# Performance work log

Hardware: AMD Instinct MI355X
Metric: run time of the kernel (lower is better)

The kernel has to match this reference:

```python
import jax, jax.numpy as jnp
import numpy as np

D_MODEL = 768
NUM_HEADS = 12


def setup_inputs() -> dict:
    key = jax.random.key(0)
    ks = jax.random.split(key, 11)
    B, N, D = 4, 2048, D_MODEL
    s = 1.0 / np.sqrt(D)
    return {
        "q": jax.random.normal(ks[0], (B, N, D), jnp.float32),
        "k": jax.random.normal(ks[1], (B, N, D), jnp.float32),
        "v": jax.random.normal(ks[2], (B, N, D), jnp.float32),
        "wq": jax.random.normal(ks[3], (D, D), jnp.float32) * s,
        "bq": jnp.zeros((D,), jnp.float32),
        "wk": jax.random.normal(ks[4], (D, D), jnp.float32) * s,
        "bk": jnp.zeros((D,), jnp.float32),
        "wv": jax.random.normal(ks[5], (D, D), jnp.float32) * s,
        "bv": jnp.zeros((D,), jnp.float32),
        "wo": jax.random.normal(ks[6], (D, D), jnp.float32) * s,
        "bo": jnp.zeros((D,), jnp.float32),
    }


def _split_heads(x, num_heads):
    B, N, D = x.shape
    hd = D // num_heads
    return x.reshape(B, N, num_heads, hd).transpose(0, 2, 1, 3)  # (B,H,N,hd)


def reference(q, k, v, wq, bq, wk, bk, wv, bv, wo, bo):
    B, N, D = q.shape
    H = NUM_HEADS
    qw = q @ wq.T + bq
    kw = k @ wk.T + bk
    vw = v @ wv.T + bv
    hq = _split_heads(qw, H)
    hk = _split_heads(kw, H)
    hv = _split_heads(vw, H)
    scale = 1.0 / jnp.sqrt(jnp.asarray(hq.shape[-1], hq.dtype))
    scores = jnp.einsum("bhnd,bhmd->bhnm", hq, hk) * scale  # (B,H,N,N) explicit
    attn = jax.nn.softmax(scores, axis=-1)
    out = jnp.einsum("bhnm,bhmd->bhnd", attn, hv)
    out = out.transpose(0, 2, 1, 3).reshape(B, N, D)
    return out @ wo.T + bo
```

## Files before the change

### kernel.cpp

```cpp
#include <hip/hip_runtime.h>
#include <hip/hip_bf16.h>
#include <type_traits>


typedef __attribute__((ext_vector_type(8)))  __bf16 bf16x8;
typedef __attribute__((ext_vector_type(4)))  __bf16 bf16x4;
typedef __attribute__((ext_vector_type(4)))  float  f32x4;
typedef __attribute__((ext_vector_type(16))) float  f32x16;
typedef __attribute__((ext_vector_type(2)))  unsigned u32x2;
typedef __attribute__((ext_vector_type(4)))  unsigned u32x4;

#define NH  12
#define HD  64
#define DM  768
#define SEQ 2048
#define NB  4
#define M8  8192
#define ALPHA 0.18033688011112043f

__device__ __forceinline__ f32x4 mfma16(bf16x8 a, bf16x8 b, f32x4 c) {
  return __builtin_amdgcn_mfma_f32_16x16x32_bf16(a, b, c, 0, 0, 0);
}
__device__ __forceinline__ f32x16 mfma32(bf16x8 a, bf16x8 b, f32x16 c) {
  return __builtin_amdgcn_mfma_f32_32x32x16_bf16(a, b, c, 0, 0, 0);
}
__device__ __forceinline__ void gload16(const void* g, void* l) {
  auto gp = (__attribute__((address_space(1))) void*)(const_cast<void*>(g));
  auto lp = (__attribute__((address_space(3))) void*)(l);
  __builtin_amdgcn_global_load_lds(gp, lp, 16, 0, 0);
}
__device__ __forceinline__ float exp2_(float x) {
#if __has_builtin(__builtin_amdgcn_exp2f)
  return __builtin_amdgcn_exp2f(x);
#else
  return exp2f(x);
#endif
}

#define VMLG(n) do { asm volatile("s_waitcnt vmcnt(" #n ") lgkmcnt(0)" ::: "memory"); \
                     __builtin_amdgcn_sched_barrier(0); } while (0)
#define VMW(n) do { asm volatile("s_waitcnt vmcnt(" #n ")" ::: "memory"); \
                    __builtin_amdgcn_sched_barrier(0); } while (0)
#define BARX do { __builtin_amdgcn_s_barrier(); \
                  __builtin_amdgcn_sched_barrier(0); } while (0)

__device__ __forceinline__ u32x2 pswap(unsigned a, unsigned b) {
#if __has_builtin(__builtin_amdgcn_permlane32_swap)
  return __builtin_amdgcn_permlane32_swap(a, b, false, false);
#else
  u32x2 r;
  unsigned sa = (unsigned)__shfl_xor((int)a, 32), sb = (unsigned)__shfl_xor((int)b, 32);
  int hi = ((int)threadIdx.x >> 5) & 1;
  r[0] = hi ? sb : a;
  r[1] = hi ? b : sa;
  return r;
#endif
}
__device__ __forceinline__ unsigned f2u(float x) { return __builtin_bit_cast(unsigned, x); }
__device__ __forceinline__ float    u2f(unsigned x) { return __builtin_bit_cast(float, x); }
__device__ __forceinline__ float pcomb_sum(float v) {
  u32x2 r = pswap(f2u(v), f2u(v));
  return u2f(r[0]) + u2f(r[1]);
}
__device__ __forceinline__ unsigned pk(float lo, float hi_) {
  unsigned short ua = __builtin_bit_cast(unsigned short, (__bf16)lo);
  unsigned short ub = __builtin_bit_cast(unsigned short, (__bf16)hi_);
  return ((unsigned)ub << 16) | ua;
}

__global__ void cast4_kernel(const float* __restrict__ a, const float* __restrict__ b,
                             const float* __restrict__ c, const float* __restrict__ d,
                             __bf16* __restrict__ oa, __bf16* __restrict__ ob,
                             __bf16* __restrict__ oc, __bf16* __restrict__ od, int n4) {
  int y = blockIdx.y;
  const float* in = y == 0 ? a : y == 1 ? b : y == 2 ? c : d;
  __bf16* out     = y == 0 ? oa : y == 1 ? ob : y == 2 ? oc : od;
  const float sc  = y == 0 ? ALPHA : 1.0f;
  int i = blockIdx.x * 256 + threadIdx.x;
  if (i < n4) {
    float4 v = ((const float4*)in)[i];
    bf16x4 r;
    r[0] = (__bf16)(v.x * sc); r[1] = (__bf16)(v.y * sc);
    r[2] = (__bf16)(v.z * sc); r[3] = (__bf16)(v.w * sc);
    ((bf16x4*)out)[i] = r;
  }
}

__device__ __forceinline__ void proj_body(const float* __restrict__ A,
                                          const __bf16* __restrict__ B,
                                          const float* __restrict__ bias,
                                          __bf16* __restrict__ C,
                                          long m0, long n0, float bscale, bool trans) {
  __shared__ __align__(16) char LDSG[32768];
  const int tid = threadIdx.x;
  const int w = tid >> 6, l = tid & 63;
  const int g = l >> 4, i16 = l & 15;
  const int wr = w >> 1, wc = w & 1;
  const int srow = l >> 2;
  const int kq = l & 3;
  const int swc = kq ^ ((srow >> 1) & 3);

  const __bf16* Bg = B + (n0 + 16 * w + srow) * (long)DM + swc * 8;
  const float*  Ag = A + (m0 + 16 * w + srow) * (long)DM + kq * 8;
  char* const Awr = LDSG + w * 1024 + srow * 64 + swc * 16;

  const int chsw = (g ^ ((i16 >> 1) & 3)) * 16;
  const char* fA = LDSG + (wr * 64 + i16) * 64 + chsw;
  const char* fB = LDSG + 16384 + (wc * 64 + i16) * 64 + chsw;

  f32x4 acc[4][4] = {};
  float4 arA[4], arB[4];
  long kAa = 0, kAb = 32, kB = 0;

  auto LAA = [&]() {
    arA[0] = *(const float4*)(Ag + kAa);
    arA[1] = *(const float4*)(Ag + kAa + 4);
    arA[2] = *(const float4*)(Ag + 64 * (long)DM + kAa);
    arA[3] = *(const float4*)(Ag + 64 * (long)DM + kAa + 4);
    kAa += 64;
  };
  auto LAB = [&]() {
    arB[0] = *(const float4*)(Ag + kAb);
    arB[1] = *(const float4*)(Ag + kAb + 4);
    arB[2] = *(const float4*)(Ag + 64 * (long)DM + kAb);
    arB[3] = *(const float4*)(Ag + 64 * (long)DM + kAb + 4);
    kAb += 64;
  };
  auto SB = [&](int selb) {
    gload16(Bg + kB, LDSG + 16384 + selb + w * 1024);
    gload16(Bg + 64 * (long)DM + kB, LDSG + 16384 + selb + w * 1024 + 4096);
    kB += 32;
  };
  auto WAA = [&](int selb) {
    u32x4 u0, u1;
    u0[0] = pk(arA[0].x, arA[0].y); u0[1] = pk(arA[0].z, arA[0].w);
    u0[2] = pk(arA[1].x, arA[1].y); u0[3] = pk(arA[1].z, arA[1].w);
    u1[0] = pk(arA[2].x, arA[2].y); u1[1] = pk(arA[2].z, arA[2].w);
    u1[2] = pk(arA[3].x, arA[3].y); u1[3] = pk(arA[3].z, arA[3].w);
    *(u32x4*)(Awr + selb) = u0;
    *(u32x4*)(Awr + selb + 4096) = u1;
  };
  auto WAB = [&](int selb) {
    u32x4 u0, u1;
    u0[0] = pk(arB[0].x, arB[0].y); u0[1] = pk(arB[0].z, arB[0].w);
    u0[2] = pk(arB[1].x, arB[1].y); u0[3] = pk(arB[1].z, arB[1].w);
    u1[0] = pk(arB[2].x, arB[2].y); u1[1] = pk(arB[2].z, arB[2].w);
    u1[2] = pk(arB[3].x, arB[3].y); u1[3] = pk(arB[3].z, arB[3].w);
    *(u32x4*)(Awr + selb) = u0;
    *(u32x4*)(Awr + selb + 4096) = u1;
  };

#define PCOMPUTE(SELB) do { \
    bf16x8 af[4], bfr[4]; \
    _Pragma("unroll") for (int m = 0; m < 4; ++m) \
      af[m] = *(const bf16x8*)(fA + (SELB) + m * 1024); \
    _Pragma("unroll") for (int n = 0; n < 4; ++n) \
      bfr[n] = *(const bf16x8*)(fB + (SELB) + n * 1024); \
    __builtin_amdgcn_s_setprio(1); \
    _Pragma("unroll") for (int m = 0; m < 4; ++m) \
      _Pragma("unroll") for (int n = 0; n < 4; ++n) \
        acc[m][n] = mfma16(af[m], bfr[n], acc[m][n]); \
    __builtin_amdgcn_s_setprio(0); } while (0)

  SB(0); LAA(); LAB(); WAA(0);
  asm volatile("s_waitcnt lgkmcnt(0)" ::: "memory");
  __builtin_amdgcn_sched_barrier(0);
  BARX;
#pragma unroll 1
  for (int j = 0; j < 11; ++j) {
    SB(8192); LAA(); PCOMPUTE(0);    WAB(8192); VMLG(4); BARX;
    SB(0);    LAB(); PCOMPUTE(8192); WAA(0);    VMLG(4); BARX;
  }
  SB(8192); PCOMPUTE(0); WAB(8192); VMLG(0); BARX;
  PCOMPUTE(8192);
#undef PCOMPUTE

  if (trans) {
#pragma unroll
    for (int m = 0; m < 4; ++m)
#pragma unroll
      for (int n = 0; n < 4; ++n) {
        const long col = n0 + wc * 64 + n * 16 + i16;
        const float bv = bias[col] * bscale;
        const long row0 = m0 + wr * 64 + m * 16 + g * 4;
        bf16x4 v4;
#pragma unroll
        for (int r = 0; r < 4; ++r) v4[r] = (__bf16)(acc[m][n][r] + bv);
        *(bf16x4*)(C + col * (long)M8 + row0) = v4;
      }
  } else {
#pragma unroll
    for (int m = 0; m < 4; ++m)
#pragma unroll
      for (int n = 0; n < 4; ++n) {
        const long col = n0 + wc * 64 + n * 16 + i16;
        const float bv = bias[col] * bscale;
        const long row0 = m0 + wr * 64 + m * 16 + g * 4;
#pragma unroll
        for (int r = 0; r < 4; ++r)
          C[(row0 + r) * DM + col] = (__bf16)(acc[m][n][r] + bv);
      }
  }
}

__global__ __launch_bounds__(256, 3) void proj3_gemm(
    const float* __restrict__ q, const float* __restrict__ k, const float* __restrict__ v,
    const __bf16* __restrict__ wqb, const __bf16* __restrict__ wkb, const __bf16* __restrict__ wvb,
    const float* __restrict__ bq, const float* __restrict__ bk, const float* __restrict__ bv,
    __bf16* __restrict__ qpj, __bf16* __restrict__ kpj, __bf16* __restrict__ vpT) {
  const int gid = blockIdx.x;
  const int swz = (gid & 7) * 144 + (gid >> 3);
  const int z = swz / 384, rem = swz % 384;
  const long xb = rem / 6, yb = rem % 6;
  const float* A = z == 0 ? q : z == 1 ? k : v;
  const __bf16* B = z == 0 ? wqb : z == 1 ? wkb : wvb;
  const float* bias = z == 0 ? bq : z == 1 ? bk : bv;
  __bf16* C = z == 0 ? qpj : z == 1 ? kpj : vpT;
  proj_body(A, B, bias, C, xb * 128, yb * 128, z == 0 ? ALPHA : 1.0f, z == 2);
}

__global__ __launch_bounds__(256) void out_gemm(const __bf16* __restrict__ A,
                                                const __bf16* __restrict__ B,
                                                const float* __restrict__ bias,
                                                float* __restrict__ C) {
  const int gid = blockIdx.x;
  const int swz = (gid & 7) * 48 + (gid >> 3);
  const long m0 = (swz / 6) * 128, n0 = (swz % 6) * 128;

  __shared__ __align__(16) char LDSG[32768];
  const int tid = threadIdx.x;
  const int w = tid >> 6, l = tid & 63;
  const int g = l >> 4, i16 = l & 15;
  const int wr = w >> 1, wc = w & 1;
  const int srow = l >> 2;
  const int swc = (l & 3) ^ ((srow >> 1) & 3);
  const __bf16* Ag = A + (m0 + 16 * w + srow) * (long)DM + swc * 8;
  const __bf16* Bg = B + (n0 + 16 * w + srow) * (long)DM + swc * 8;
  const int chsw = (g ^ ((i16 >> 1) & 3)) * 16;
  const char* fA = LDSG + (wr * 64 + i16) * 64 + chsw;
  const char* fB = LDSG + 16384 + (wc * 64 + i16) * 64 + chsw;

  f32x4 acc[4][4] = {};
  long kB = 0;

#define GSTAGE(SELB) do { \
    gload16(Ag + kB, LDSG + (SELB) + w * 1024); \
    gload16(Ag + 64 * (long)DM + kB, LDSG + (SELB) + w * 1024 + 4096); \
    gload16(Bg + kB, LDSG + 16384 + (SELB) + w * 1024); \
    gload16(Bg + 64 * (long)DM + kB, LDSG + 16384 + (SELB) + w * 1024 + 4096); \
    kB += 32; } while (0)

#define GCOMPUTE(SELB) do { \
    bf16x8 af[4], bfr[4]; \
    _Pragma("unroll") for (int m = 0; m < 4; ++m) \
      af[m] = *(const bf16x8*)(fA + (SELB) + m * 1024); \
    _Pragma("unroll") for (int n = 0; n < 4; ++n) \
      bfr[n] = *(const bf16x8*)(fB + (SELB) + n * 1024); \
    __builtin_amdgcn_s_setprio(1); \
    _Pragma("unroll") for (int m = 0; m < 4; ++m) \
      _Pragma("unroll") for (int n = 0; n < 4; ++n) \
        acc[m][n] = mfma16(af[m], bfr[n], acc[m][n]); \
    __builtin_amdgcn_s_setprio(0); } while (0)

  GSTAGE(0); GSTAGE(8192);
#pragma unroll 1
  for (int k = 0; k + 128 <= DM; k += 64) {
    VMW(4); BARX; GCOMPUTE(0);    BARX; GSTAGE(0);
    VMW(4); BARX; GCOMPUTE(8192); BARX; GSTAGE(8192);
  }
  VMW(4); BARX; GCOMPUTE(0);
  VMW(0); BARX; GCOMPUTE(8192);
#undef GSTAGE
#undef GCOMPUTE

#pragma unroll
  for (int m = 0; m < 4; ++m)
#pragma unroll
    for (int n = 0; n < 4; ++n) {
      const long col = n0 + wc * 64 + n * 16 + i16;
      const float bv = bias[col];
      const long row0 = m0 + wr * 64 + m * 16 + g * 4;
#pragma unroll
      for (int r = 0; r < 4; ++r)
        C[(row0 + r) * DM + col] = acc[m][n][r] + bv;
    }
}

__global__ __launch_bounds__(256) void attn_fwd(const __bf16* __restrict__ qp,
                                                const __bf16* __restrict__ kp,
                                                const __bf16* __restrict__ vpT,
                                                __bf16* __restrict__ ao) {
  __shared__ __align__(16) __bf16 Ks[2][64 * 64];
  __shared__ __align__(16) __bf16 Vs[2][64 * 64];

  const int wg = blockIdx.x;
  const int xcd = wg & 7;
  const int idx = wg >> 3;
  const int bh = xcd * 6 + (idx >> 4);
  const int qt = idx & 15;
  const int b = bh / NH, h = bh % NH;

  const int tid = threadIdx.x;
  const int w = tid >> 6, l = tid & 63;
  const int l31 = l & 31, hi = l >> 5;

  const long qrow = (long)b * SEQ + qt * 128 + w * 32 + l31;
  const __bf16* qb = qp + qrow * DM + h * HD;
  bf16x8 qf[4];
#pragma unroll
  for (int kk = 0; kk < 4; ++kk) qf[kk] = *(const bf16x8*)(qb + kk * 16 + hi * 8);

  f32x16 o0 = {}, o1 = {};
  float lsum = 0.f;

  const int srow = tid >> 3;
  const int schunk = (tid & 7) ^ (srow & 7);
  const __bf16* kbase = kp + ((long)b * SEQ) * DM + h * HD;
  const __bf16* vtb = vpT + (long)(h * HD) * M8 + (long)b * SEQ;

  auto stage = [&](int T, int sel) {
    const long kt = (long)T * 64;
    __bf16* Kd = &Ks[sel][(w * 8) * 64];
    __bf16* Vd = &Vs[sel][(w * 8) * 64];
    gload16(kbase + (kt + srow) * (long)DM + schunk * 8, Kd);
    gload16(kbase + (kt + 32 + srow) * (long)DM + schunk * 8, Kd + 32 * 64);
    gload16(vtb + (long)srow * M8 + kt + schunk * 8, Vd);
    gload16(vtb + (long)(32 + srow) * M8 + kt + schunk * 8, Vd + 32 * 64);
  };

  auto compute = [&](const __bf16* Kc, const __bf16* Vc) {
    f32x16 s0 = {}, s1 = {};
    __builtin_amdgcn_s_setprio(1);
#pragma unroll
    for (int kk = 0; kk < 4; ++kk) {
      const int cl = kk * 2 + hi;
      bf16x8 kf0 = *(const bf16x8*)&Kc[l31 * 64 + ((cl ^ (l31 & 7)) * 8)];
      s0 = mfma32(kf0, qf[kk], s0);
      bf16x8 kf1 = *(const bf16x8*)&Kc[(32 + l31) * 64 + ((cl ^ (l31 & 7)) * 8)];
      s1 = mfma32(kf1, qf[kk], s1);
    }
    __builtin_amdgcn_s_setprio(0);

#pragma unroll
    for (int r = 0; r < 16; ++r) s0[r] = exp2_(s0[r]);
#pragma unroll
    for (int r = 0; r < 16; ++r) s1[r] = exp2_(s1[r]);
    f32x16 ps = s0 + s1;
    const float t0 = (ps[0] + ps[1]) + (ps[2] + ps[3]);
    const float t1 = (ps[4] + ps[5]) + (ps[6] + ps[7]);
    const float t2 = (ps[8] + ps[9]) + (ps[10] + ps[11]);
    const float t3 = (ps[12] + ps[13]) + (ps[14] + ps[15]);
    lsum += (t0 + t1) + (t2 + t3);

    bf16x8 pf[4];
#pragma unroll
    for (int ks = 0; ks < 4; ++ks) {
      const int base = 8 * (ks & 1);
      const f32x16& S = (ks < 2) ? s0 : s1;
      unsigned pa = pk(S[base + 0], S[base + 1]);
      unsigned pc = pk(S[base + 2], S[base + 3]);
      unsigned pb = pk(S[base + 4], S[base + 5]);
      unsigned pd = pk(S[base + 6], S[base + 7]);
      u32x2 r02 = pswap(pa, pb);
      u32x2 r13 = pswap(pc, pd);
      u32x4 pw;
      pw[0] = r02[0]; pw[1] = r13[0]; pw[2] = r02[1]; pw[3] = r13[1];
      pf[ks] = __builtin_bit_cast(bf16x8, pw);
    }

    __builtin_amdgcn_s_setprio(1);
#pragma unroll
    for (int ks = 0; ks < 4; ++ks) {
      const int cl = ks * 2 + hi;
      bf16x8 vf0 = *(const bf16x8*)&Vc[l31 * 64 + ((cl ^ (l31 & 7)) * 8)];
      o0 = mfma32(vf0, pf[ks], o0);
      bf16x8 vf1 = *(const bf16x8*)&Vc[(32 + l31) * 64 + ((cl ^ (l31 & 7)) * 8)];
      o1 = mfma32(vf1, pf[ks], o1);
    }
    __builtin_amdgcn_s_setprio(0);
  };

  stage(0, 0);
  __syncthreads();
  for (int t = 0; t < SEQ / 64; t += 2) {
    if (t + 1 < SEQ / 64) stage(t + 1, 1);
    compute(Ks[0], Vs[0]);
    __syncthreads();
    if (t + 2 < SEQ / 64) stage(t + 2, 0);
    compute(Ks[1], Vs[1]);
    __syncthreads();
  }

  const float inv = 1.0f / pcomb_sum(lsum);
  __bf16* obase = ao + qrow * DM + h * HD;
#pragma unroll
  for (int rg = 0; rg < 4; ++rg) {
    bf16x4 v0, v1;
#pragma unroll
    for (int j = 0; j < 4; ++j) {
      v0[j] = (__bf16)(o0[rg * 4 + j] * inv);
      v1[j] = (__bf16)(o1[rg * 4 + j] * inv);
    }
    *(bf16x4*)(obase + 8 * rg + 4 * hi) = v0;
    *(bf16x4*)(obase + 32 + 8 * rg + 4 * hi) = v1;
  }
}

extern "C" void kernel_launch(void* const* d_in, const int* in_sizes, int n_in,
                              void* d_out, int out_size, void* d_ws, size_t ws_size,
                              hipStream_t stream) {
  const float* q  = (const float*)d_in[0];
  const float* k  = (const float*)d_in[1];
  const float* v  = (const float*)d_in[2];
  const float* wq = (const float*)d_in[3];
  const float* bq = (const float*)d_in[4];
  const float* wk = (const float*)d_in[5];
  const float* bk = (const float*)d_in[6];
  const float* wv = (const float*)d_in[7];
  const float* bv = (const float*)d_in[8];
  const float* wo = (const float*)d_in[9];
  const float* bo = (const float*)d_in[10];

  const long S = (long)M8 * DM;
  const long W = (long)DM * DM;
  __bf16* ws = (__bf16*)d_ws;
  __bf16 *wqb = ws, *wkb = wqb + W, *wvb = wkb + W, *wob = wvb + W;
  __bf16 *qpj = wob + W, *kpj = qpj + S, *vpT = kpj + S, *aob = vpT + S;

  cast4_kernel<<<dim3((unsigned)(W / 4 / 256), 4), 256, 0, stream>>>(
      wq, wk, wv, wo, wqb, wkb, wvb, wob, (int)(W / 4));

  proj3_gemm<<<1152, 256, 0, stream>>>(q, k, v, wqb, wkb, wvb, bq, bk, bv, qpj, kpj, vpT);

  attn_fwd<<<768, 256, 0, stream>>>(qpj, kpj, vpT, aob);

  out_gemm<<<384, 256, 0, stream>>>(aob, wob, bo, (float*)d_out);
}
```

Measured before the change: 153.2 us.

## Give each attention wave two 32-row query tiles, halving threads per block

The attention kernel now runs 2 waves of 128 threads per block instead of 4. Each wave handles 64 query rows as two 32-row MFMA tiles that share each K and V fragment read from LDS, which halves the LDS reads per MFMA. The staging loop is reworked so 128 threads still fill the same 64x64 K/V tiles. The cost is roughly double the accumulator and score registers per wave and fewer waves per block to hide latency.

Measured after the change: 152.9 us. About the same (-0.2%).

```diff
diff --git a/kernel.cpp b/kernel.cpp
--- a/kernel.cpp
+++ b/kernel.cpp
@@ -286,10 +286,10 @@
     }
 }
 
-__global__ __launch_bounds__(256) void attn_fwd(const __bf16* __restrict__ qp,
-                                                const __bf16* __restrict__ kp,
-                                                const __bf16* __restrict__ vpT,
-                                                __bf16* __restrict__ ao) {
+__global__ __launch_bounds__(128, 2) void attn_fwd(const __bf16* __restrict__ qp,
+                                                   const __bf16* __restrict__ kp,
+                                                   const __bf16* __restrict__ vpT,
+                                                   __bf16* __restrict__ ao) {
   __shared__ __align__(16) __bf16 Ks[2][64 * 64];
   __shared__ __align__(16) __bf16 Vs[2][64 * 64];
 
@@ -304,14 +304,17 @@
   const int w = tid >> 6, l = tid & 63;
   const int l31 = l & 31, hi = l >> 5;
 
-  const long qrow = (long)b * SEQ + qt * 128 + w * 32 + l31;
-  const __bf16* qb = qp + qrow * DM + h * HD;
-  bf16x8 qf[4];
-#pragma unroll
-  for (int kk = 0; kk < 4; ++kk) qf[kk] = *(const bf16x8*)(qb + kk * 16 + hi * 8);
-
-  f32x16 o0 = {}, o1 = {};
-  float lsum = 0.f;
+  const long qrow0 = (long)b * SEQ + qt * 128 + w * 64 + l31;
+  const __bf16* qb0 = qp + qrow0 * DM + h * HD;
+  bf16x8 qf0[4], qf1[4];
+#pragma unroll
+  for (int kk = 0; kk < 4; ++kk) {
+    qf0[kk] = *(const bf16x8*)(qb0 + kk * 16 + hi * 8);
+    qf1[kk] = *(const bf16x8*)(qb0 + 32 * DM + kk * 16 + hi * 8);
+  }
+
+  f32x16 o00 = {}, o01 = {}, o10 = {}, o11 = {};
+  float lsum0 = 0.f, lsum1 = 0.f;
 
   const int srow = tid >> 3;
   const int schunk = (tid & 7) ^ (srow & 7);
@@ -320,62 +323,95 @@
 
   auto stage = [&](int T, int sel) {
     const long kt = (long)T * 64;
-    __bf16* Kd = &Ks[sel][(w * 8) * 64];
-    __bf16* Vd = &Vs[sel][(w * 8) * 64];
-    gload16(kbase + (kt + srow) * (long)DM + schunk * 8, Kd);
-    gload16(kbase + (kt + 32 + srow) * (long)DM + schunk * 8, Kd + 32 * 64);
-    gload16(vtb + (long)srow * M8 + kt + schunk * 8, Vd);
-    gload16(vtb + (long)(32 + srow) * M8 + kt + schunk * 8, Vd + 32 * 64);
+    __bf16* Kd = &Ks[sel][w * 512];
+    __bf16* Vd = &Vs[sel][w * 512];
+#pragma unroll
+    for (int j = 0; j < 4; ++j) {
+      gload16(kbase + (kt + 16 * j + srow) * (long)DM + schunk * 8, Kd + j * 1024);
+      gload16(vtb + (long)(16 * j + srow) * M8 + kt + schunk * 8, Vd + j * 1024);
+    }
   };
 
   auto compute = [&](const __bf16* Kc, const __bf16* Vc) {
-    f32x16 s0 = {}, s1 = {};
+    f32x16 s00 = {}, s01 = {}, s10 = {}, s11 = {};
     __builtin_amdgcn_s_setprio(1);
 #pragma unroll
     for (int kk = 0; kk < 4; ++kk) {
-      const int cl = kk * 2 + hi;
-      bf16x8 kf0 = *(const bf16x8*)&Kc[l31 * 64 + ((cl ^ (l31 & 7)) * 8)];
-      s0 = mfma32(kf0, qf[kk], s0);
-      bf16x8 kf1 = *(const bf16x8*)&Kc[(32 + l31) * 64 + ((cl ^ (l31 & 7)) * 8)];
-      s1 = mfma32(kf1, qf[kk], s1);
+      const int sw = ((kk * 2 + hi) ^ (l31 & 7)) * 8;
+      bf16x8 kf0 = *(const bf16x8*)&Kc[l31 * 64 + sw];
+      s00 = mfma32(kf0, qf0[kk], s00);
+      s10 = mfma32(kf0, qf1[kk], s10);
+      bf16x8 kf1 = *(const bf16x8*)&Kc[2048 + l31 * 64 + sw];
+      s01 = mfma32(kf1, qf0[kk], s01);
+      s11 = mfma32(kf1, qf1[kk], s11);
     }
     __builtin_amdgcn_s_setprio(0);
 
 #pragma unroll
-    for (int r = 0; r < 16; ++r) s0[r] = exp2_(s0[r]);
-#pragma unroll
-    for (int r = 0; r < 16; ++r) s1[r] = exp2_(s1[r]);
-    f32x16 ps = s0 + s1;
-    const float t0 = (ps[0] + ps[1]) + (ps[2] + ps[3]);
-    const float t1 = (ps[4] + ps[5]) + (ps[6] + ps[7]);
-    const float t2 = (ps[8] + ps[9]) + (ps[10] + ps[11]);
-    const float t3 = (ps[12] + ps[13]) + (ps[14] + ps[15]);
-    lsum += (t0 + t1) + (t2 + t3);
-
-    bf16x8 pf[4];
+    for (int r = 0; r < 16; ++r) s00[r] = exp2_(s00[r]);
+#pragma unroll
+    for (int r = 0; r < 16; ++r) s01[r] = exp2_(s01[r]);
+#pragma unroll
+    for (int r = 0; r < 16; ++r) s10[r] = exp2_(s10[r]);
+#pragma unroll
+    for (int r = 0; r < 16; ++r) s11[r] = exp2_(s11[r]);
+    {
+      f32x16 ps = s00 + s01;
+      const float t0 = (ps[0] + ps[1]) + (ps[2] + ps[3]);
+      const float t1 = (ps[4] + ps[5]) + (ps[6] + ps[7]);
+      const float t2 = (ps[8] + ps[9]) + (ps[10] + ps[11]);
+      const float t3 = (ps[12] + ps[13]) + (ps[14] + ps[15]);
+      lsum0 += (t0 + t1) + (t2 + t3);
+    }
+    {
+      f32x16 ps = s10 + s11;
+      const float t0 = (ps[0] + ps[1]) + (ps[2] + ps[3]);
+      const float t1 = (ps[4] + ps[5]) + (ps[6] + ps[7]);
+      const float t2 = (ps[8] + ps[9]) + (ps[10] + ps[11]);
+      const float t3 = (ps[12] + ps[13]) + (ps[14] + ps[15]);
+      lsum1 += (t0 + t1) + (t2 + t3);
+    }
+
+    bf16x8 pf0[4], pf1[4];
 #pragma unroll
     for (int ks = 0; ks < 4; ++ks) {
       const int base = 8 * (ks & 1);
-      const f32x16& S = (ks < 2) ? s0 : s1;
-      unsigned pa = pk(S[base + 0], S[base + 1]);
-      unsigned pc = pk(S[base + 2], S[base + 3]);
-      unsigned pb = pk(S[base + 4], S[base + 5]);
-      unsigned pd = pk(S[base + 6], S[base + 7]);
-      u32x2 r02 = pswap(pa, pb);
-      u32x2 r13 = pswap(pc, pd);
-      u32x4 pw;
-      pw[0] = r02[0]; pw[1] = r13[0]; pw[2] = r02[1]; pw[3] = r13[1];
-      pf[ks] = __builtin_bit_cast(bf16x8, pw);
+      {
+        const f32x16& S = (ks < 2) ? s00 : s01;
+        unsigned pa = pk(S[base + 0], S[base + 1]);
+        unsigned pc = pk(S[base + 2], S[base + 3]);
+        unsigned pb = pk(S[base + 4], S[base + 5]);
+        unsigned pd = pk(S[base + 6], S[base + 7]);
+        u32x2 r02 = pswap(pa, pb);
+        u32x2 r13 = pswap(pc, pd);
+        u32x4 pw;
+        pw[0] = r02[0]; pw[1] = r13[0]; pw[2] = r02[1]; pw[3] = r13[1];
+        pf0[ks] = __builtin_bit_cast(bf16x8, pw);
+      }
+      {
+        const f32x16& S = (ks < 2) ? s10 : s11;
+        unsigned pa = pk(S[base + 0], S[base + 1]);
+        unsigned pc = pk(S[base + 2], S[base + 3]);
+        unsigned pb = pk(S[base + 4], S[base + 5]);
+        unsigned pd = pk(S[base + 6], S[base + 7]);
+        u32x2 r02 = pswap(pa, pb);
+        u32x2 r13 = pswap(pc, pd);
+        u32x4 pw;
+        pw[0] = r02[0]; pw[1] = r13[0]; pw[2] = r02[1]; pw[3] = r13[1];
+        pf1[ks] = __builtin_bit_cast(bf16x8, pw);
+      }
     }
 
     __builtin_amdgcn_s_setprio(1);
 #pragma unroll
     for (int ks = 0; ks < 4; ++ks) {
-      const int cl = ks * 2 + hi;
-      bf16x8 vf0 = *(const bf16x8*)&Vc[l31 * 64 + ((cl ^ (l31 & 7)) * 8)];
-      o0 = mfma32(vf0, pf[ks], o0);
-      bf16x8 vf1 = *(const bf16x8*)&Vc[(32 + l31) * 64 + ((cl ^ (l31 & 7)) * 8)];
-      o1 = mfma32(vf1, pf[ks], o1);
+      const int sw = ((ks * 2 + hi) ^ (l31 & 7)) * 8;
+      bf16x8 vf0 = *(const bf16x8*)&Vc[l31 * 64 + sw];
+      o00 = mfma32(vf0, pf0[ks], o00);
+      o10 = mfma32(vf0, pf1[ks], o10);
+      bf16x8 vf1 = *(const bf16x8*)&Vc[2048 + l31 * 64 + sw];
+      o01 = mfma32(vf1, pf0[ks], o01);
+      o11 = mfma32(vf1, pf1[ks], o11);
     }
     __builtin_amdgcn_s_setprio(0);
   };
@@ -391,18 +427,24 @@
     __syncthreads();
   }
 
-  const float inv = 1.0f / pcomb_sum(lsum);
-  __bf16* obase = ao + qrow * DM + h * HD;
+  const float inv0 = 1.0f / pcomb_sum(lsum0);
+  const float inv1 = 1.0f / pcomb_sum(lsum1);
+  __bf16* ob0 = ao + qrow0 * DM + h * HD;
+  __bf16* ob1 = ob0 + 32 * DM;
 #pragma unroll
   for (int rg = 0; rg < 4; ++rg) {
-    bf16x4 v0, v1;
+    bf16x4 a0, a1, b0, b1;
 #pragma unroll
     for (int j = 0; j < 4; ++j) {
-      v0[j] = (__bf16)(o0[rg * 4 + j] * inv);
-      v1[j] = (__bf16)(o1[rg * 4 + j] * inv);
-    }
-    *(bf16x4*)(obase + 8 * rg + 4 * hi) = v0;
-    *(bf16x4*)(obase + 32 + 8 * rg + 4 * hi) = v1;
+      a0[j] = (__bf16)(o00[rg * 4 + j] * inv0);
+      a1[j] = (__bf16)(o01[rg * 4 + j] * inv0);
+      b0[j] = (__bf16)(o10[rg * 4 + j] * inv1);
+      b1[j] = (__bf16)(o11[rg * 4 + j] * inv1);
+    }
+    *(bf16x4*)(ob0 + 8 * rg + 4 * hi) = a0;
+    *(bf16x4*)(ob0 + 32 + 8 * rg + 4 * hi) = a1;
+    *(bf16x4*)(ob1 + 8 * rg + 4 * hi) = b0;
+    *(bf16x4*)(ob1 + 32 + 8 * rg + 4 * hi) = b1;
   }
 }
 
@@ -432,7 +474,7 @@
 
   proj3_gemm<<<1152, 256, 0, stream>>>(q, k, v, wqb, wkb, wvb, bq, bk, bv, qpj, kpj, vpT);
 
-  attn_fwd<<<768, 256, 0, stream>>>(qpj, kpj, vpT, aob);
+  attn_fwd<<<768, 128, 0, stream>>>(qpj, kpj, vpT, aob);
 
   out_gemm<<<384, 256, 0, stream>>>(aob, wob, bo, (float*)d_out);
 }
```

## Software-pipeline PV matmul with next QK in attention; shrink out-GEMM tiles

Applied to the files above, without the earlier changes.

The attention loop is restructured so that the PV MFMAs for tile t-1 run in the same MFMA block as the QK MFMAs for tile t. This interleaves matrix work with the exp/pack softmax step, and V fragments are held in registers across iterations. A launch-bounds occupancy hint of 3 waves is added. The output GEMM switches to 64x128 tiles with 768 blocks to fill more CUs, at the cost of less reuse per block. Keeping extra fragments live raises register pressure, which may conflict with the occupancy target.

After: 148.5 us (median of 2 runs). 1.03x faster.

```diff
diff --git a/kernel.cpp b/kernel.cpp
--- a/kernel.cpp
+++ b/kernel.cpp
@@ -224,10 +224,12 @@
                                                 const float* __restrict__ bias,
                                                 float* __restrict__ C) {
   const int gid = blockIdx.x;
-  const int swz = (gid & 7) * 48 + (gid >> 3);
-  const long m0 = (swz / 6) * 128, n0 = (swz % 6) * 128;
-
-  __shared__ __align__(16) char LDSG[32768];
+  const int local = (gid >> 3);
+  const long mt = (gid & 7) * 16 + local / 6;
+  const long nt = local % 6;
+  const long m0 = mt * 64, n0 = nt * 128;
+
+  __shared__ __align__(16) char LDSG[24576];
   const int tid = threadIdx.x;
   const int w = tid >> 6, l = tid & 63;
   const int g = l >> 4, i16 = l & 15;
@@ -237,59 +239,58 @@
   const __bf16* Ag = A + (m0 + 16 * w + srow) * (long)DM + swc * 8;
   const __bf16* Bg = B + (n0 + 16 * w + srow) * (long)DM + swc * 8;
   const int chsw = (g ^ ((i16 >> 1) & 3)) * 16;
-  const char* fA = LDSG + (wr * 64 + i16) * 64 + chsw;
-  const char* fB = LDSG + 16384 + (wc * 64 + i16) * 64 + chsw;
-
-  f32x4 acc[4][4] = {};
+  const char* fA = LDSG + (wr * 32 + i16) * 64 + chsw;
+  const char* fB = LDSG + 8192 + (wc * 64 + i16) * 64 + chsw;
+
+  f32x4 acc[2][4] = {};
   long kB = 0;
 
-#define GSTAGE(SELB) do { \
-    gload16(Ag + kB, LDSG + (SELB) + w * 1024); \
-    gload16(Ag + 64 * (long)DM + kB, LDSG + (SELB) + w * 1024 + 4096); \
-    gload16(Bg + kB, LDSG + 16384 + (SELB) + w * 1024); \
-    gload16(Bg + 64 * (long)DM + kB, LDSG + 16384 + (SELB) + w * 1024 + 4096); \
+#define GSTAGE(S) do { \
+    gload16(Ag + kB, LDSG + (S) * 4096 + w * 1024); \
+    gload16(Bg + kB, LDSG + 8192 + (S) * 8192 + w * 1024); \
+    gload16(Bg + 64 * (long)DM + kB, LDSG + 8192 + (S) * 8192 + w * 1024 + 4096); \
     kB += 32; } while (0)
 
-#define GCOMPUTE(SELB) do { \
-    bf16x8 af[4], bfr[4]; \
-    _Pragma("unroll") for (int m = 0; m < 4; ++m) \
-      af[m] = *(const bf16x8*)(fA + (SELB) + m * 1024); \
+#define GCOMPUTE(S) do { \
+    bf16x8 af[2], bfr[4]; \
+    _Pragma("unroll") for (int m = 0; m < 2; ++m) \
+      af[m] = *(const bf16x8*)(fA + (S) * 4096 + m * 1024); \
     _Pragma("unroll") for (int n = 0; n < 4; ++n) \
-      bfr[n] = *(const bf16x8*)(fB + (SELB) + n * 1024); \
+      bfr[n] = *(const bf16x8*)(fB + (S) * 8192 + n * 1024); \
     __builtin_amdgcn_s_setprio(1); \
-    _Pragma("unroll") for (int m = 0; m < 4; ++m) \
+    _Pragma("unroll") for (int m = 0; m < 2; ++m) \
       _Pragma("unroll") for (int n = 0; n < 4; ++n) \
         acc[m][n] = mfma16(af[m], bfr[n], acc[m][n]); \
     __builtin_amdgcn_s_setprio(0); } while (0)
 
-  GSTAGE(0); GSTAGE(8192);
+  GSTAGE(0); GSTAGE(1);
 #pragma unroll 1
   for (int k = 0; k + 128 <= DM; k += 64) {
-    VMW(4); BARX; GCOMPUTE(0);    BARX; GSTAGE(0);
-    VMW(4); BARX; GCOMPUTE(8192); BARX; GSTAGE(8192);
-  }
-  VMW(4); BARX; GCOMPUTE(0);
-  VMW(0); BARX; GCOMPUTE(8192);
+    VMW(3); BARX; GCOMPUTE(0); BARX; GSTAGE(0);
+    VMW(3); BARX; GCOMPUTE(1); BARX; GSTAGE(1);
+  }
+  VMW(3); BARX; GCOMPUTE(0);
+  VMW(0); BARX; GCOMPUTE(1);
 #undef GSTAGE
 #undef GCOMPUTE
 
 #pragma unroll
-  for (int m = 0; m < 4; ++m)
+  for (int m = 0; m < 2; ++m)
 #pragma unroll
     for (int n = 0; n < 4; ++n) {
       const long col = n0 + wc * 64 + n * 16 + i16;
       const float bv = bias[col];
-      const long row0 = m0 + wr * 64 + m * 16 + g * 4;
+      const long row0 = m0 + wr * 32 + m * 16 + g * 4;
 #pragma unroll
       for (int r = 0; r < 4; ++r)
         C[(row0 + r) * DM + col] = acc[m][n][r] + bv;
     }
 }
 
-__global__ __launch_bounds__(256) void attn_fwd(const __bf16* __restrict__ qp,
-                                                const __bf16* __restrict__ kp,
-                                                const __bf16* __restrict__ vpT,
-                                                __bf16* __restrict__ ao) {
+__global__ __launch_bounds__(256, 3) void attn_fwd(const __bf16* __restrict__ qp,
+                                                   const __bf16* __restrict__ kp,
+                                                   const __bf16* __restrict__ vpT,
+                                                   __bf16* __restrict__ ao) {
   __shared__ __align__(16) __bf16 Ks[2][64 * 64];
   __shared__ __align__(16) __bf16 Vs[2][64 * 64];
 
@@ -312,6 +313,7 @@
 
   f32x16 o0 = {}, o1 = {};
   float lsum = 0.f;
+  bf16x8 vfp[8], pfp[4];
 
   const int srow = tid >> 3;
   const int schunk = (tid & 7) ^ (srow & 7);
@@ -328,19 +330,40 @@
     gload16(vtb + (long)(32 + srow) * M8 + kt + schunk * 8, Vd + 32 * 64);
   };
 
-  auto compute = [&](const __bf16* Kc, const __bf16* Vc) {
-    f32x16 s0 = {}, s1 = {};
+  auto qk = [&](const __bf16* Kc, f32x16& s0, f32x16& s1, bool pv) {
+    bf16x8 kf[8];
+#pragma unroll
+    for (int kk = 0; kk < 4; ++kk) {
+      const int sw = ((kk * 2 + hi) ^ (l31 & 7)) * 8;
+      kf[kk]     = *(const bf16x8*)&Kc[l31 * 64 + sw];
+      kf[4 + kk] = *(const bf16x8*)&Kc[2048 + l31 * 64 + sw];
+    }
     __builtin_amdgcn_s_setprio(1);
+    if (pv) {
+#pragma unroll
+      for (int ks = 0; ks < 4; ++ks) {
+        o0 = mfma32(vfp[ks], pfp[ks], o0);
+        o1 = mfma32(vfp[4 + ks], pfp[ks], o1);
+      }
+    }
 #pragma unroll
     for (int kk = 0; kk < 4; ++kk) {
-      const int cl = kk * 2 + hi;
-      bf16x8 kf0 = *(const bf16x8*)&Kc[l31 * 64 + ((cl ^ (l31 & 7)) * 8)];
-      s0 = mfma32(kf0, qf[kk], s0);
-      bf16x8 kf1 = *(const bf16x8*)&Kc[(32 + l31) * 64 + ((cl ^ (l31 & 7)) * 8)];
-      s1 = mfma32(kf1, qf[kk], s1);
+      s0 = mfma32(kf[kk], qf[kk], s0);
+      s1 = mfma32(kf[4 + kk], qf[kk], s1);
     }
     __builtin_amdgcn_s_setprio(0);
-
+  };
+
+  auto load_v = [&](const __bf16* Vc) {
+#pragma unroll
+    for (int ks = 0; ks < 4; ++ks) {
+      const int sw = ((ks * 2 + hi) ^ (l31 & 7)) * 8;
+      vfp[ks]     = *(const bf16x8*)&Vc[l31 * 64 + sw];
+      vfp[4 + ks] = *(const bf16x8*)&Vc[2048 + l31 * 64 + sw];
+    }
+  };
+
+  auto softmax_pack = [&](f32x16& s0, f32x16& s1) {
 #pragma unroll
     for (int r = 0; r < 16; ++r) s0[r] = exp2_(s0[r]);
 #pragma unroll
@@ -351,8 +374,6 @@
     const float t2 = (ps[8] + ps[9]) + (ps[10] + ps[11]);
     const float t3 = (ps[12] + ps[13]) + (ps[14] + ps[15]);
     lsum += (t0 + t1) + (t2 + t3);
-
-    bf16x8 pf[4];
 #pragma unroll
     for (int ks = 0; ks < 4; ++ks) {
       const int base = 8 * (ks & 1);
@@ -365,30 +386,38 @@
       u32x2 r13 = pswap(pc, pd);
       u32x4 pw;
       pw[0] = r02[0]; pw[1] = r13[0]; pw[2] = r02[1]; pw[3] = r13[1];
-      pf[ks] = __builtin_bit_cast(bf16x8, pw);
-    }
-
+      pfp[ks] = __builtin_bit_cast(bf16x8, pw);
+    }
+  };
+
+  stage(0, 0);
+  stage(1, 1);
+  __syncthreads();
+  {
+    f32x16 s0 = {}, s1 = {};
+    qk(&Ks[0][0], s0, s1, false);
+    load_v(&Vs[0][0]);
+    softmax_pack(s0, s1);
+    __syncthreads();
+  }
+#pragma unroll 1
+  for (int t = 1; t < SEQ / 64; ++t) {
+    const int sel = t & 1;
+    if (t + 1 < SEQ / 64) stage(t + 1, sel ^ 1);
+    f32x16 s0 = {}, s1 = {};
+    qk(&Ks[sel][0], s0, s1, true);
+    load_v(&Vs[sel][0]);
+    softmax_pack(s0, s1);
+    __syncthreads();
+  }
+  {
     __builtin_amdgcn_s_setprio(1);
 #pragma unroll
     for (int ks = 0; ks < 4; ++ks) {
-      const int cl = ks * 2 + hi;
-      bf16x8 vf0 = *(const bf16x8*)&Vc[l31 * 64 + ((cl ^ (l31 & 7)) * 8)];
-      o0 = mfma32(vf0, pf[ks], o0);
-      bf16x8 vf1 = *(const bf16x8*)&Vc[(32 + l31) * 64 + ((cl ^ (l31 & 7)) * 8)];
-      o1 = mfma32(vf1, pf[ks], o1);
+      o0 = mfma32(vfp[ks], pfp[ks], o0);
+      o1 = mfma32(vfp[4 + ks], pfp[ks], o1);
     }
     __builtin_amdgcn_s_setprio(0);
-  };
-
-  stage(0, 0);
-  __syncthreads();
-  for (int t = 0; t < SEQ / 64; t += 2) {
-    if (t + 1 < SEQ / 64) stage(t + 1, 1);
-    compute(Ks[0], Vs[0]);
-    __syncthreads();
-    if (t + 2 < SEQ / 64) stage(t + 2, 0);
-    compute(Ks[1], Vs[1]);
-    __syncthreads();
   }
 
   const float inv = 1.0f / pcomb_sum(lsum);
@@ -434,5 +463,5 @@
 
   attn_fwd<<<768, 256, 0, stream>>>(qpj, kpj, vpT, aob);
 
-  out_gemm<<<384, 256, 0, stream>>>(aob, wob, bo, (float*)d_out);
-}
+  out_gemm<<<768, 256, 0, stream>>>(aob, wob, bo, (float*)d_out);
+}
```
